# Performance work log

Hardware: AMD Instinct MI355X
Metric: run time of the kernel (lower is better)

The kernel has to match this reference:

```python
import jax, jax.numpy as jnp
import numpy as np
import math

G = 256      # graphs per batch
N0 = 256     # nodes per graph at input
RATIO = 0.5  # TopKPooling ratio


def gcn_conv(x, src, dst, ew, W, b):
    h = x @ W
    n = x.shape[0]
    deg = jnp.zeros((n,), x.dtype).at[dst].add(ew) + 1.0  # +1 for self-loop
    dinv = jax.lax.rsqrt(deg)
    norm = dinv[src] * dinv[dst] * ew
    agg = jnp.zeros_like(h).at[dst].add(norm[:, None] * h[src])
    return agg + h / deg[:, None] + b  # self-loop norm = 1/deg


def topk_pool(x, src, dst, ew, w, n_per_graph):
    # PyG TopKPooling: score = tanh(x.w/||w||); keep top ceil(ratio*n) per graph;
    # x_out = x[perm] * score[perm]; edges between dropped nodes are masked out.
    k = int(math.ceil(RATIO * n_per_graph))
    score = jnp.tanh((x @ w) / jnp.linalg.norm(w))
    top_s, top_i = jax.lax.top_k(score.reshape(G, n_per_graph), k)  # [G,k]
    perm = (top_i + (jnp.arange(G) * n_per_graph)[:, None]).reshape(-1)
    new_x = x[perm] * top_s.reshape(-1, 1)
    new_id = jnp.full((x.shape[0],), -1, jnp.int32).at[perm].set(
        jnp.arange(G * k, dtype=jnp.int32))
    ns, nd = new_id[src], new_id[dst]
    valid = (ns >= 0) & (nd >= 0)
    new_ew = ew * valid.astype(x.dtype)
    ns = jnp.where(valid, ns, 0)
    nd = jnp.where(valid, nd, 0)
    new_batch = jnp.repeat(jnp.arange(G, dtype=jnp.int32), k)
    return new_x, ns, nd, new_ew, new_batch, k


def readout(x, batch):
    # torch.cat([global_max_pool, global_mean_pool], dim=1)
    mx = jax.ops.segment_max(x, batch, num_segments=G)
    cnt = jax.ops.segment_sum(jnp.ones((x.shape[0],), x.dtype), batch, num_segments=G)
    mn = jax.ops.segment_sum(x, batch, num_segments=G) / cnt[:, None]
    return jnp.concatenate([mx, mn], axis=1)


def _forward(x, edge_index, batch, gcn_w0, gcn_b0, gcn_w1, gcn_b1, gcn_w2, gcn_b2,
             pool_w0, pool_w1, pool_w2, lin1_w, lin1_b, lin2_w, lin2_b, lin3_w, lin3_b):
    src, dst = edge_index[0], edge_index[1]
    ew = jnp.ones((src.shape[0],), x.dtype)
    npg = N0
    h = jax.nn.relu(gcn_conv(x, src, dst, ew, gcn_w0, gcn_b0))
    h, src, dst, ew, batch, npg = topk_pool(h, src, dst, ew, pool_w0, npg)
    out = readout(h, batch)
    for Wg, bg, pw in ((gcn_w1, gcn_b1, pool_w1), (gcn_w2, gcn_b2, pool_w2)):
        h = jax.nn.relu(gcn_conv(h, src, dst, ew, Wg, bg))
        h, src, dst, ew, batch, npg = topk_pool(h, src, dst, ew, pw, npg)
        out = out + readout(h, batch)
    h1 = jax.nn.relu(out @ lin1_w + lin1_b)  # dropout = identity (eval mode)
    h2 = jax.nn.relu(h1 @ lin2_w + lin2_b)
    logits = h2 @ lin3_w + lin3_b
    return jax.nn.log_softmax(logits, axis=-1)


def setup_inputs() -> dict:
    key = jax.random.key(0)
    ks = jax.random.split(key, 16)
    EPG = 2048  # edges per graph (avg degree 8)
    F_IN, H = 128, 256
    num_nodes, E = G * N0, G * EPG
    x = jax.random.normal(ks[0], (num_nodes, F_IN), jnp.float32)
    offs = jnp.repeat(jnp.arange(G, dtype=jnp.int32) * N0, EPG)
    src = offs + jax.random.randint(ks[1], (E,), 0, N0, dtype=jnp.int32)
    dst = offs + jax.random.randint(ks[2], (E,), 0, N0, dtype=jnp.int32)

    def glorot(k, shape):
        lim = float(np.sqrt(6.0 / (shape[0] + shape[1])))
        return jax.random.uniform(k, shape, jnp.float32, -lim, lim)

    return {
        "x": x,
        "edge_index": jnp.stack([src, dst]),
        "batch": jnp.arange(num_nodes, dtype=jnp.int32) // N0,
        "gcn_w0": glorot(ks[3], (F_IN, H)), "gcn_b0": jnp.zeros((H,), jnp.float32),
        "gcn_w1": glorot(ks[4], (H, H)), "gcn_b1": jnp.zeros((H,), jnp.float32),
        "gcn_w2": glorot(ks[5], (H, H)), "gcn_b2": jnp.zeros((H,), jnp.float32),
        "pool_w0": jax.random.normal(ks[6], (H,), jnp.float32) * 0.1,
        "pool_w1": jax.random.normal(ks[7], (H,), jnp.float32) * 0.1,
        "pool_w2": jax.random.normal(ks[8], (H,), jnp.float32) * 0.1,
        "lin1_w": glorot(ks[9], (2 * H, H)), "lin1_b": jnp.zeros((H,), jnp.float32),
        "lin2_w": glorot(ks[10], (H, H // 2)), "lin2_b": jnp.zeros((H // 2,), jnp.float32),
        "lin3_w": glorot(ks[11], (H // 2, 2)), "lin3_b": jnp.zeros((2,), jnp.float32),
    }


def reference(x, edge_index, batch, gcn_w0, gcn_b0, gcn_w1, gcn_b1, gcn_w2, gcn_b2,
              pool_w0, pool_w1, pool_w2, lin1_w, lin1_b, lin2_w, lin2_b, lin3_w, lin3_b):
    return _forward(x, edge_index, batch, gcn_w0, gcn_b0, gcn_w1, gcn_b1, gcn_w2, gcn_b2,
                    pool_w0, pool_w1, pool_w2, lin1_w, lin1_b, lin2_w, lin2_b, lin3_w, lin3_b)
```

## Files before the change

kernel.cpp:

```cpp
#include <hip/hip_runtime.h>
#include <hip/hip_bf16.h>
#include <math.h>

#define G_GRAPHS 256
#define EPG 2048
#define E_TOT 524288
#define HF 256
#define FIN 128

__global__ void init_cur(int* __restrict__ cur) {
    int i = blockIdx.x * blockDim.x + threadIdx.x;
    if (i < G_GRAPHS * 256) cur[i] = i & 255;
}

template <int K>
__global__ __launch_bounds__(256, 4)
void gemm_v9(const float* __restrict__ A, const float* __restrict__ W,
             float* __restrict__ C) {
    __shared__ __align__(16) float As[2][32 * 68];
    __shared__ __align__(16) float Wa[2][32 * 68];
    __shared__ __align__(16) float Wb[2][32 * 68];
    const int tid = threadIdx.x;
    const int tx = tid & 15;
    const int ty = tid >> 4;
    const int r0 = blockIdx.x * 64;
    const int c0 = blockIdx.y * 128;
    const int l8 = tid >> 3;
    const int kq = tid & 7;
    const int wkk = tid >> 5;
    const int wc = tid & 31;
    float acc[4][8] = {{0.f}};
    float4 va0, va1, vw0, vw1, vw2, vw3;

    auto load_regs = [&](int k0) {
        va0 = *(const float4*)&A[(size_t)(r0 + l8) * K + k0 + 4 * kq];
        va1 = *(const float4*)&A[(size_t)(r0 + 32 + l8) * K + k0 + 4 * kq];
        vw0 = *(const float4*)&W[(size_t)(k0 + 0  + wkk) * 256 + c0 + 4 * wc];
        vw1 = *(const float4*)&W[(size_t)(k0 + 8  + wkk) * 256 + c0 + 4 * wc];
        vw2 = *(const float4*)&W[(size_t)(k0 + 16 + wkk) * 256 + c0 + 4 * wc];
        vw3 = *(const float4*)&W[(size_t)(k0 + 24 + wkk) * 256 + c0 + 4 * wc];
    };
    auto write_stage = [&](int b) {
        {
            int rs = l8 ^ (kq << 3);
            As[b][(4 * kq + 0) * 68 + rs] = va0.x;
            As[b][(4 * kq + 1) * 68 + rs] = va0.y;
            As[b][(4 * kq + 2) * 68 + rs] = va0.z;
            As[b][(4 * kq + 3) * 68 + rs] = va0.w;
        }
        {
            int rs = (32 + l8) ^ (kq << 3);
            As[b][(4 * kq + 0) * 68 + rs] = va1.x;
            As[b][(4 * kq + 1) * 68 + rs] = va1.y;
            As[b][(4 * kq + 2) * 68 + rs] = va1.z;
            As[b][(4 * kq + 3) * 68 + rs] = va1.w;
        }
        if (wc < 16) {
            *(float4*)&Wa[b][(0  + wkk) * 68 + 4 * wc] = vw0;
            *(float4*)&Wa[b][(8  + wkk) * 68 + 4 * wc] = vw1;
            *(float4*)&Wa[b][(16 + wkk) * 68 + 4 * wc] = vw2;
            *(float4*)&Wa[b][(24 + wkk) * 68 + 4 * wc] = vw3;
        } else {
            *(float4*)&Wb[b][(0  + wkk) * 68 + 4 * (wc - 16)] = vw0;
            *(float4*)&Wb[b][(8  + wkk) * 68 + 4 * (wc - 16)] = vw1;
            *(float4*)&Wb[b][(16 + wkk) * 68 + 4 * (wc - 16)] = vw2;
            *(float4*)&Wb[b][(24 + wkk) * 68 + 4 * (wc - 16)] = vw3;
        }
    };
    auto compute = [&](int b) {
#pragma unroll 4
        for (int kk = 0; kk < 32; ++kk) {
            const int g = (ty * 4) ^ ((kk >> 2) << 3);
            const float4 a0 = *(const float4*)&As[b][kk * 68 + g];
            const float4 w0 = *(const float4*)&Wa[b][kk * 68 + tx * 4];
            const float4 w1 = *(const float4*)&Wb[b][kk * 68 + tx * 4];
            float av[4] = {a0.x, a0.y, a0.z, a0.w};
            float wv_[8] = {w0.x, w0.y, w0.z, w0.w, w1.x, w1.y, w1.z, w1.w};
#pragma unroll
            for (int i = 0; i < 4; ++i)
#pragma unroll
                for (int j = 0; j < 8; ++j)
                    acc[i][j] += av[i] * wv_[j];
        }
    };

    load_regs(0);
    write_stage(0);
    __syncthreads();
    int cur = 0;
    for (int k0 = 0; k0 < K - 32; k0 += 32) {
        load_regs(k0 + 32);
        compute(cur);
        write_stage(cur ^ 1);
        __syncthreads();
        cur ^= 1;
    }
    compute(cur);

#pragma unroll
    for (int i = 0; i < 4; ++i) {
        float4 v0 = make_float4(acc[i][0], acc[i][1], acc[i][2], acc[i][3]);
        float4 v1 = make_float4(acc[i][4], acc[i][5], acc[i][6], acc[i][7]);
        size_t base = (size_t)(r0 + ty * 4 + i) * 256 + c0 + tx * 4;
        *(float4*)&C[base] = v0;
        *(float4*)&C[base + 64] = v1;
    }
}

__global__ __launch_bounds__(256)
void csr_build(const int* __restrict__ ei, const int* __restrict__ cur, int npg,
               int* __restrict__ degS, float* __restrict__ dinvS,
               int* __restrict__ startsS, int2* __restrict__ slots2) {
    __shared__ int cul[EPG];
    __shared__ short dstv[EPG];
    __shared__ unsigned char rnk[EPG];
    __shared__ int h[32][256];
    __shared__ int cnt[256];
    __shared__ int st[256];
    const int g = blockIdx.x;
    const int t = threadIdx.x;
    const int lane = t & 63;
    const int wv = t >> 6;

    for (int i = t; i < 32 * 256; i += 256) ((int*)h)[i] = 0;
    for (int e = t; e < EPG; e += 256) {
        size_t idx = (size_t)g * EPG + e;
        int cu = cur[g * 256 + (ei[idx] - g * 256)];
        int cv = cur[g * 256 + (ei[E_TOT + idx] - g * 256)];
        bool valid = (cu >= 0 && cv >= 0);
        cul[e] = cu;
        dstv[e] = valid ? (short)cv : (short)256;
    }
    __syncthreads();
    for (int c = wv; c < 32; c += 4) {
        int e = c * 64 + lane;
        int d = (int)dstv[e];
        unsigned long long m = ~0ULL;
#pragma unroll
        for (int b = 0; b < 9; ++b) {
            unsigned long long bb = __ballot((d >> b) & 1);
            m &= ((d >> b) & 1) ? bb : ~bb;
        }
        int r = __popcll(m & ((1ULL << lane) - 1ULL));
        rnk[e] = (unsigned char)r;
        if (r == 0 && d < 256) h[c][d] = __popcll(m);
    }
    __syncthreads();
    if (t < npg) {
        int run = 0;
        for (int c = 0; c < 32; ++c) { int v = h[c][t]; h[c][t] = run; run += v; }
        cnt[t] = run;
        degS[g * npg + t] = run + 1;
        dinvS[g * npg + t] = 1.0f / sqrtf((float)(run + 1));
    }
    __syncthreads();
    if (t == 0) {
        int run = 0;
        for (int i = 0; i < npg; ++i) { st[i] = run; run += cnt[i]; }
    }
    __syncthreads();
    if (t < npg) startsS[g * npg + t] = g * EPG + st[t];
    for (int e = t; e < EPG; e += 256) {
        int d = (int)dstv[e];
        if (d < npg) {
            int slot = st[d] + h[e >> 6][d] + (int)rnk[e];
            int cu = cul[e];
            float dv = 1.0f / sqrtf((float)(cnt[cu] + 1));
            slots2[g * EPG + slot] = make_int2(g * npg + cu, __float_as_int(dv));
        }
    }
}

__global__ __launch_bounds__(256)
void agg_score2(const int* __restrict__ degS, const float* __restrict__ dinvS,
                const int* __restrict__ startsS, const int2* __restrict__ slots2,
                const float* __restrict__ HL, float* __restrict__ H2,
                const float* __restrict__ bias, const float* __restrict__ pw,
                float* __restrict__ score, int nbOver8) {
    __shared__ float vrow[4][256];
    const int t = threadIdx.x;
    const int wv = t >> 6;
    const int lane = t & 63;
    const int blk = (blockIdx.x & 7) * nbOver8 + (blockIdx.x >> 3);
    const int node = blk * 4 + wv;
    const int cntE = degS[node] - 1;
    const float degF = (float)(cntE + 1);
    const float dn = dinvS[node];
    const int2* sl = slots2 + startsS[node];
    float ax = 0.f, ay = 0.f, az = 0.f, aw = 0.f;
    int j = 0;
    for (; j + 8 <= cntE; j += 8) {
        int2 s[8];
#pragma unroll
        for (int u = 0; u < 8; ++u) s[u] = sl[j + u];
        float4 hv[8];
#pragma unroll
        for (int u = 0; u < 8; ++u)
            hv[u] = *(const float4*)&HL[(size_t)s[u].x * 256 + 4 * lane];
#pragma unroll
        for (int u = 0; u < 8; ++u) {
            float dv = __int_as_float(s[u].y);
            ax += dv * hv[u].x; ay += dv * hv[u].y;
            az += dv * hv[u].z; aw += dv * hv[u].w;
        }
    }
    for (; j + 4 <= cntE; j += 4) {
        int2 s[4];
#pragma unroll
        for (int u = 0; u < 4; ++u) s[u] = sl[j + u];
        float4 hv[4];
#pragma unroll
        for (int u = 0; u < 4; ++u)
            hv[u] = *(const float4*)&HL[(size_t)s[u].x * 256 + 4 * lane];
#pragma unroll
        for (int u = 0; u < 4; ++u) {
            float dv = __int_as_float(s[u].y);
            ax += dv * hv[u].x; ay += dv * hv[u].y;
            az += dv * hv[u].z; aw += dv * hv[u].w;
        }
    }
    for (; j < cntE; ++j) {
        int2 sv = sl[j];
        float dv = __int_as_float(sv.y);
        float4 hv = *(const float4*)&HL[(size_t)sv.x * 256 + 4 * lane];
        ax += dv * hv.x; ay += dv * hv.y; az += dv * hv.z; aw += dv * hv.w;
    }
    const float4 hn = *(const float4*)&HL[(size_t)node * 256 + 4 * lane];
    const float4 bi = *(const float4*)&bias[4 * lane];
    float4 v;
    v.x = ax * dn + hn.x / degF + bi.x;  v.x = fmaxf(v.x, 0.f);
    v.y = ay * dn + hn.y / degF + bi.y;  v.y = fmaxf(v.y, 0.f);
    v.z = az * dn + hn.z / degF + bi.z;  v.z = fmaxf(v.z, 0.f);
    v.w = aw * dn + hn.w / degF + bi.w;  v.w = fmaxf(v.w, 0.f);
    *(float4*)&H2[(size_t)node * 256 + 4 * lane] = v;
    *(float4*)&vrow[wv][4 * lane] = v;
    float pr = 0.f, s2p = 0.f;
    for (int jj = 0; jj < 4; ++jj) {
        int f = lane + 64 * jj;
        float w = pw[f];
        pr += vrow[wv][f] * w;
        s2p += w * w;
    }
    for (int off = 32; off; off >>= 1) {
        pr += __shfl_down(pr, off, 64);
        s2p += __shfl_down(s2p, off, 64);
    }
    s2p = __shfl(s2p, 0, 64);
    if (lane == 0) score[node] = tanhf(pr / sqrtf(s2p));
}

__global__ __launch_bounds__(256)
void topk_fused(const float* __restrict__ score, int npg, int k,
                const float* __restrict__ H2, float* __restrict__ OUT,
                float* __restrict__ outacc, int* __restrict__ cur, int first) {
    __shared__ float ss[256];
    __shared__ int si_[256];
    __shared__ int rankOf[256];
    const int g = blockIdx.x;
    const int t = threadIdx.x;
    if (t < npg) { ss[t] = score[g * npg + t]; si_[t] = t; }
    else         { ss[t] = -INFINITY; si_[t] = 0x7FFFFFFF; }
    for (int size = 2; size <= 256; size <<= 1) {
        for (int stride = size >> 1; stride > 0; stride >>= 1) {
            __syncthreads();
            int i = t, j = t ^ stride;
            if (j > i) {
                float a = ss[i], b = ss[j];
                int ia = si_[i], ib = si_[j];
                bool inOrder = (a > b) || (a == b && ia < ib);
                bool desc = ((i & size) == 0);
                if (desc ? !inOrder : inOrder) {
                    ss[i] = b; ss[j] = a; si_[i] = ib; si_[j] = ia;
                }
            }
        }
    }
    __syncthreads();
    rankOf[t] = -1;
    __syncthreads();
    if (t < k) rankOf[si_[t]] = t;
    __syncthreads();
    {
        int v = g * 256 + t;
        int c = cur[v];
        cur[v] = (c >= 0) ? rankOf[c] : -1;
    }
    const size_t gb = (size_t)g * npg * 256;
    float mx = -INFINITY, sm = 0.f;
    for (int n = 0; n < k; n += 4) {
        float v0 = H2[gb + (size_t)si_[n + 0] * 256 + t] * ss[n + 0];
        float v1 = H2[gb + (size_t)si_[n + 1] * 256 + t] * ss[n + 1];
        float v2 = H2[gb + (size_t)si_[n + 2] * 256 + t] * ss[n + 2];
        float v3 = H2[gb + (size_t)si_[n + 3] * 256 + t] * ss[n + 3];
        size_t ob = ((size_t)g * k + n) * 256 + t;
        OUT[ob]       = v0;
        OUT[ob + 256] = v1;
        OUT[ob + 512] = v2;
        OUT[ob + 768] = v3;
        mx = fmaxf(mx, v0); sm += v0;
        mx = fmaxf(mx, v1); sm += v1;
        mx = fmaxf(mx, v2); sm += v2;
        mx = fmaxf(mx, v3); sm += v3;
    }
    float mean = sm / (float)k;
    if (first) {
        outacc[g * 512 + t] = mx;
        outacc[g * 512 + 256 + t] = mean;
    } else {
        outacc[g * 512 + t] += mx;
        outacc[g * 512 + 256 + t] += mean;
    }
}

__global__ __launch_bounds__(256)
void mlp_head(const float* __restrict__ outacc,
              const float* __restrict__ l1w, const float* __restrict__ l1b,
              const float* __restrict__ l2w, const float* __restrict__ l2b,
              const float* __restrict__ l3w, const float* __restrict__ l3b,
              float* __restrict__ out) {
    __shared__ float row[512];
    __shared__ float h1[256];
    __shared__ float h2[128];
    const int g = blockIdx.x;
    const int t = threadIdx.x;
    row[t] = outacc[g * 512 + t];
    row[256 + t] = outacc[g * 512 + 256 + t];
    __syncthreads();
    {
        float a = l1b[t];
        for (int j = 0; j < 512; ++j) a += row[j] * l1w[j * 256 + t];
        h1[t] = fmaxf(a, 0.f);
    }
    __syncthreads();
    if (t < 128) {
        float a2 = l2b[t];
        for (int j = 0; j < 256; ++j) a2 += h1[j] * l2w[j * 128 + t];
        h2[t] = fmaxf(a2, 0.f);
    }
    __syncthreads();
    if (t == 0) {
        float l0 = l3b[0], l1 = l3b[1];
        for (int j = 0; j < 128; ++j) {
            float h = h2[j];
            l0 += h * l3w[j * 2 + 0];
            l1 += h * l3w[j * 2 + 1];
        }
        float m = fmaxf(l0, l1);
        float lse = m + logf(expf(l0 - m) + expf(l1 - m));
        out[g * 2 + 0] = l0 - lse;
        out[g * 2 + 1] = l1 - lse;
    }
}

__global__ __launch_bounds__(256, 1)
void gnn_mono(const float* __restrict__ x, const int* __restrict__ ei,
              const float* __restrict__ gw0, const float* __restrict__ gb0,
              const float* __restrict__ gw1, const float* __restrict__ gb1,
              const float* __restrict__ gw2, const float* __restrict__ gb2,
              const float* __restrict__ pw0, const float* __restrict__ pw1,
              const float* __restrict__ pw2,
              const float* __restrict__ l1w, const float* __restrict__ l1b,
              const float* __restrict__ l2w, const float* __restrict__ l2b,
              const float* __restrict__ l3w, const float* __restrict__ l3b,
              float* __restrict__ out, float* __restrict__ ws) {
    const int g = blockIdx.x;
    const int t = threadIdx.x;
    float* P = ws + (size_t)g * HF * 256;
    float* Q = ws + (size_t)G_GRAPHS * HF * 256 + (size_t)g * HF * 256;
    __shared__ int   eb[EPG];
    __shared__ int   slots[EPG];
    __shared__ int   curID[256];
    __shared__ int   cntL[256];
    __shared__ int   startL[256];
    __shared__ float degF[256];
    __shared__ float dinv[256];
    __shared__ float sa[256];
    __shared__ float ss[256];
    __shared__ int   si_[256];
    __shared__ float scoreV[256];
    __shared__ int   kept[128];
    __shared__ int   rankOf[256];
    __shared__ float row[512];
    for (int e = t; e < EPG; e += 256) {
        size_t idx = (size_t)g * EPG + e;
        eb[e] = ((ei[idx] - g * 256) << 8) | (ei[E_TOT + idx] - g * 256);
    }
    curID[t] = t;
    float accMx = 0.f, accMn = 0.f;
    const float* GW[3] = {gw0, gw1, gw2};
    const float* GB[3] = {gb0, gb1, gb2};
    const float* PW[3] = {pw0, pw1, pw2};
    const int kk[3] = {128, 64, 32};
    int npg = 256;
    __syncthreads();
    for (int s = 0; s < 3; ++s) {
        const int knext = kk[s];
        {
            const float* Wp = GW[s];
            const int K = (s == 0) ? FIN : HF;
            for (int n = 0; n < npg; ++n) {
                if (s == 0) { if (t < FIN) sa[t] = x[(size_t)(g * 256 + n) * FIN + t]; }
                else sa[t] = P[(size_t)n * HF + t];
                __syncthreads();
                float a = 0.f;
                for (int k2 = 0; k2 < K; ++k2) a += sa[k2] * Wp[k2 * HF + t];
                Q[(size_t)n * HF + t] = a;
                __syncthreads();
            }
        }
        cntL[t] = 0;
        __syncthreads();
        for (int e = t; e < EPG; e += 256) {
            int p = eb[e];
            int cu = curID[p >> 8], cv = curID[p & 255];
            if (cu >= 0 && cv >= 0) atomicAdd(&cntL[cv], 1);
        }
        __syncthreads();
        if (t == 0) { int run = 0; for (int i = 0; i < npg; ++i) { startL[i] = run; run += cntL[i]; } }
        __syncthreads();
        if (t < npg) {
            float d = (float)cntL[t] + 1.0f;
            degF[t] = d;
            dinv[t] = 1.0f / sqrtf(d);
            int c = startL[t];
            for (int e = 0; e < EPG; ++e) {
                int p = eb[e];
                int cu = curID[p >> 8], cv = curID[p & 255];
                if (cu >= 0 && cv >= 0 && cv == t) slots[c++] = e;
            }
        }
        __syncthreads();
        {
            const float bb = GB[s][t];
            for (int n = 0; n < npg; ++n) {
                float acc = 0.f;
                const int s0 = startL[n], s1 = s0 + cntL[n];
                for (int j = s0; j < s1; ++j) {
                    int scur = curID[eb[slots[j]] >> 8];
                    acc += dinv[scur] * Q[(size_t)scur * HF + t];
                }
                float v = acc * dinv[n] + Q[(size_t)n * HF + t] / degF[n] + bb;
                P[(size_t)n * HF + t] = fmaxf(v, 0.f);
            }
        }
        __syncthreads();
        {
            const float* pwp = PW[s];
            const int lane = t & 63, wv = t >> 6;
            float s2p = 0.f;
            for (int j = 0; j < 4; ++j) { float w = pwp[lane + 64 * j]; s2p += w * w; }
            for (int off = 32; off; off >>= 1) s2p += __shfl_down(s2p, off, 64);
            s2p = __shfl(s2p, 0, 64);
            const float nw = sqrtf(s2p);
            for (int n = wv; n < npg; n += 4) {
                float pr = 0.f;
                for (int j = 0; j < 4; ++j) { int f = lane + 64 * j; pr += P[(size_t)n * HF + f] * pwp[f]; }
                for (int off = 32; off; off >>= 1) pr += __shfl_down(pr, off, 64);
                if (lane == 0) scoreV[n] = tanhf(pr / nw);
            }
        }
        __syncthreads();
        if (t < npg) { ss[t] = scoreV[t]; si_[t] = t; }
        else         { ss[t] = -INFINITY; si_[t] = 0x7FFFFFFF; }
        for (int size = 2; size <= 256; size <<= 1) {
            for (int stride = size >> 1; stride > 0; stride >>= 1) {
                __syncthreads();
                int i = t, j = t ^ stride;
                if (j > i) {
                    float a = ss[i], b = ss[j];
                    int ia = si_[i], ib = si_[j];
                    bool inOrder = (a > b) || (a == b && ia < ib);
                    bool desc = ((i & size) == 0);
                    if (desc ? !inOrder : inOrder) { ss[i] = b; ss[j] = a; si_[i] = ib; si_[j] = ia; }
                }
            }
        }
        __syncthreads();
        if (t < knext) kept[t] = si_[t];
        __syncthreads();
        {
            float mx = -INFINITY, sm = 0.f;
            for (int n = 0; n < knext; ++n) {
                int o = kept[n];
                float vv = P[(size_t)o * HF + t] * scoreV[o];
                Q[(size_t)n * HF + t] = vv;
                mx = fmaxf(mx, vv);
                sm += vv;
            }
            accMx += mx;
            accMn += sm / (float)knext;
        }
        rankOf[t] = -1;
        __syncthreads();
        if (t < knext) rankOf[kept[t]] = t;
        __syncthreads();
        { int c = curID[t]; curID[t] = (c >= 0) ? rankOf[c] : -1; }
        __syncthreads();
        { float* tmp = P; P = Q; Q = tmp; }
        npg = knext;
    }
    row[t] = accMx;
    row[256 + t] = accMn;
    __syncthreads();
    { float a = l1b[t]; for (int j = 0; j < 512; ++j) a += row[j] * l1w[j * 256 + t]; scoreV[t] = fmaxf(a, 0.f); }
    __syncthreads();
    if (t < 128) { float a2 = l2b[t]; for (int j = 0; j < 256; ++j) a2 += scoreV[j] * l2w[j * 128 + t]; sa[t] = fmaxf(a2, 0.f); }
    __syncthreads();
    if (t == 0) {
        float l0 = l3b[0], l1 = l3b[1];
        for (int j = 0; j < 128; ++j) { float h = sa[j]; l0 += h * l3w[j * 2 + 0]; l1 += h * l3w[j * 2 + 1]; }
        float m = fmaxf(l0, l1);
        float lse = m + logf(expf(l0 - m) + expf(l1 - m));
        out[g * 2 + 0] = l0 - lse;
        out[g * 2 + 1] = l1 - lse;
    }
}

extern "C" void kernel_launch(void* const* d_in, const int* in_sizes, int n_in,
                              void* d_out, int out_size, void* d_ws, size_t ws_size,
                              hipStream_t stream) {
    const float* x   = (const float*)d_in[0];
    const int*   ei  = (const int*)d_in[1];
    const float* gw0 = (const float*)d_in[3];
    const float* gb0 = (const float*)d_in[4];
    const float* gw1 = (const float*)d_in[5];
    const float* gb1 = (const float*)d_in[6];
    const float* gw2 = (const float*)d_in[7];
    const float* gb2 = (const float*)d_in[8];
    const float* pw0 = (const float*)d_in[9];
    const float* pw1 = (const float*)d_in[10];
    const float* pw2 = (const float*)d_in[11];
    const float* l1w = (const float*)d_in[12];
    const float* l1b = (const float*)d_in[13];
    const float* l2w = (const float*)d_in[14];
    const float* l2b = (const float*)d_in[15];
    const float* l3w = (const float*)d_in[16];
    const float* l3b = (const float*)d_in[17];
    float* out = (float*)d_out;

    const size_t SLAB = (size_t)65536 * 256;
    char* p = (char*)d_ws;
    float* P      = (float*)p; p += SLAB * 4;
    float* Q      = (float*)p; p += SLAB * 4;
    int*   cur    = (int*)p;   p += (size_t)65536 * 4;
    int*   degS   = (int*)p;   p += (size_t)65536 * 4;
    float* dinvS  = (float*)p; p += (size_t)65536 * 4;
    int*   starts = (int*)p;   p += (size_t)65536 * 4;
    int2*  slots2 = (int2*)p;  p += (size_t)E_TOT * 8;
    float* score  = (float*)p; p += (size_t)65536 * 4;
    int*   kept   = (int*)p;   p += (size_t)32768 * 4;
    float* outacc = (float*)p; p += (size_t)G_GRAPHS * 512 * 4;
    const size_t needed = (size_t)(p - (char*)d_ws);

    if (ws_size < needed) {
        gnn_mono<<<G_GRAPHS, 256, 0, stream>>>(
            x, ei, gw0, gb0, gw1, gb1, gw2, gb2, pw0, pw1, pw2,
            l1w, l1b, l2w, l2b, l3w, l3b, out, (float*)d_ws);
        return;
    }

    init_cur<<<(G_GRAPHS * 256 + 255) / 256, 256, 0, stream>>>(cur);

    const int   npg[3] = {256, 128, 64};
    const int   kk[3]  = {128, 64, 32};
    const int   Ns[3]  = {65536, 32768, 16384};
    const float* GW[3] = {gw0, gw1, gw2};
    const float* GB[3] = {gb0, gb1, gb2};
    const float* PW[3] = {pw0, pw1, pw2};

    float* HLs[3]   = {P, Q, P};
    float* H2s[3]   = {Q, P, Q};
    float* POOLs[3] = {P, Q, P};

    for (int s = 0; s < 3; ++s) {
        const int n = Ns[s];
        const int k = kk[s];
        if (s == 0) {
            gemm_v9<FIN><<<dim3(n / 64, 2), 256, 0, stream>>>(x, GW[s], HLs[s]);
        } else {
            gemm_v9<HF><<<dim3(n / 64, 2), 256, 0, stream>>>(POOLs[s - 1], GW[s], HLs[s]);
        }
        csr_build<<<G_GRAPHS, 256, 0, stream>>>(ei, cur, npg[s],
                                                degS, dinvS, starts, slots2);
        agg_score2<<<n / 4, 256, 0, stream>>>(degS, dinvS, starts, slots2,
                                              HLs[s], H2s[s], GB[s], PW[s], score,
                                              n / 32);
        topk_fused<<<G_GRAPHS, 256, 0, stream>>>(score, npg[s], k,
                                                 H2s[s], POOLs[s], outacc, cur,
                                                 s == 0 ? 1 : 0);
    }

    mlp_head<<<G_GRAPHS, 256, 0, stream>>>(outacc, l1w, l1b, l2w, l2b, l3w, l3b, out);
}
```

Measured before the change: 432.0 us.

## Restructure GEMM to read wave-uniform W rows directly, staging only A in LDS

The GEMM no longer stages W tiles in shared memory. Each wave owns 32 output columns, and readfirstlane makes the W address wave-uniform, so W can be read straight from global memory, likely as scalar loads. Only A is staged, transposed, in a single double-buffered LDS tile, and each lane computes one row times 32 columns. This removes the W LDS traffic and its bank-conflict swizzling, but it relies on uniform loads being served from cache and puts 32 accumulators per thread.

```diff
diff --git a/kernel.cpp b/kernel.cpp
--- a/kernel.cpp
+++ b/kernel.cpp
@@ -15,72 +15,57 @@
 
 template <int K>
 __global__ __launch_bounds__(256, 4)
-void gemm_v9(const float* __restrict__ A, const float* __restrict__ W,
-             float* __restrict__ C) {
-    __shared__ __align__(16) float As[2][32 * 68];
-    __shared__ __align__(16) float Wa[2][32 * 68];
-    __shared__ __align__(16) float Wb[2][32 * 68];
+void gemm_v10(const float* __restrict__ A, const float* __restrict__ W,
+              float* __restrict__ C) {
+    __shared__ float As[2][32 * 68];
     const int tid = threadIdx.x;
-    const int tx = tid & 15;
-    const int ty = tid >> 4;
+    const int lane = tid & 63;
     const int r0 = blockIdx.x * 64;
-    const int c0 = blockIdx.y * 128;
-    const int l8 = tid >> 3;
-    const int kq = tid & 7;
-    const int wkk = tid >> 5;
-    const int wc = tid & 31;
-    float acc[4][8] = {{0.f}};
-    float4 va0, va1, vw0, vw1, vw2, vw3;
+    const int cb = blockIdx.y * 128 + (tid >> 6) * 32;
+    const int cbu = __builtin_amdgcn_readfirstlane(cb);
+    const float* __restrict__ Wu = W + cbu;
+    const int sr = tid >> 2;
+    const int sq = tid & 3;
+    float acc[32] = {};
+    float4 va0, va1;
 
     auto load_regs = [&](int k0) {
-        va0 = *(const float4*)&A[(size_t)(r0 + l8) * K + k0 + 4 * kq];
-        va1 = *(const float4*)&A[(size_t)(r0 + 32 + l8) * K + k0 + 4 * kq];
-        vw0 = *(const float4*)&W[(size_t)(k0 + 0  + wkk) * 256 + c0 + 4 * wc];
-        vw1 = *(const float4*)&W[(size_t)(k0 + 8  + wkk) * 256 + c0 + 4 * wc];
-        vw2 = *(const float4*)&W[(size_t)(k0 + 16 + wkk) * 256 + c0 + 4 * wc];
-        vw3 = *(const float4*)&W[(size_t)(k0 + 24 + wkk) * 256 + c0 + 4 * wc];
+        va0 = *(const float4*)&A[(size_t)(r0 + sr) * K + k0 + 4 * sq];
+        va1 = *(const float4*)&A[(size_t)(r0 + sr) * K + k0 + 16 + 4 * sq];
     };
     auto write_stage = [&](int b) {
-        {
-            int rs = l8 ^ (kq << 3);
-            As[b][(4 * kq + 0) * 68 + rs] = va0.x;
-            As[b][(4 * kq + 1) * 68 + rs] = va0.y;
-            As[b][(4 * kq + 2) * 68 + rs] = va0.z;
-            As[b][(4 * kq + 3) * 68 + rs] = va0.w;
-        }
-        {
-            int rs = (32 + l8) ^ (kq << 3);
-            As[b][(4 * kq + 0) * 68 + rs] = va1.x;
-            As[b][(4 * kq + 1) * 68 + rs] = va1.y;
-            As[b][(4 * kq + 2) * 68 + rs] = va1.z;
-            As[b][(4 * kq + 3) * 68 + rs] = va1.w;
-        }
-        if (wc < 16) {
-            *(float4*)&Wa[b][(0  + wkk) * 68 + 4 * wc] = vw0;
-            *(float4*)&Wa[b][(8  + wkk) * 68 + 4 * wc] = vw1;
-            *(float4*)&Wa[b][(16 + wkk) * 68 + 4 * wc] = vw2;
-            *(float4*)&Wa[b][(24 + wkk) * 68 + 4 * wc] = vw3;
-        } else {
-            *(float4*)&Wb[b][(0  + wkk) * 68 + 4 * (wc - 16)] = vw0;
-            *(float4*)&Wb[b][(8  + wkk) * 68 + 4 * (wc - 16)] = vw1;
-            *(float4*)&Wb[b][(16 + wkk) * 68 + 4 * (wc - 16)] = vw2;
-            *(float4*)&Wb[b][(24 + wkk) * 68 + 4 * (wc - 16)] = vw3;
-        }
+        float* p0 = &As[b][(4 * sq) * 68 + sr];
+        p0[0]   = va0.x; p0[68]  = va0.y; p0[136] = va0.z; p0[204] = va0.w;
+        float* p1 = &As[b][(16 + 4 * sq) * 68 + sr];
+        p1[0]   = va1.x; p1[68]  = va1.y; p1[136] = va1.z; p1[204] = va1.w;
     };
-    auto compute = [&](int b) {
-#pragma unroll 4
-        for (int kk = 0; kk < 32; ++kk) {
-            const int g = (ty * 4) ^ ((kk >> 2) << 3);
-            const float4 a0 = *(const float4*)&As[b][kk * 68 + g];
-            const float4 w0 = *(const float4*)&Wa[b][kk * 68 + tx * 4];
-            const float4 w1 = *(const float4*)&Wb[b][kk * 68 + tx * 4];
-            float av[4] = {a0.x, a0.y, a0.z, a0.w};
-            float wv_[8] = {w0.x, w0.y, w0.z, w0.w, w1.x, w1.y, w1.z, w1.w};
-#pragma unroll
-            for (int i = 0; i < 4; ++i)
-#pragma unroll
-                for (int j = 0; j < 8; ++j)
-                    acc[i][j] += av[i] * wv_[j];
+    auto compute = [&](int b, int k0) {
+#pragma unroll
+        for (int kq = 0; kq < 8; ++kq) {
+            float av[4];
+#pragma unroll
+            for (int u = 0; u < 4; ++u)
+                av[u] = As[b][(4 * kq + u) * 68 + lane];
+#pragma unroll
+            for (int u = 0; u < 4; ++u) {
+                const float* wr = &Wu[(size_t)(k0 + 4 * kq + u) * 256];
+                float4 w0 = *(const float4*)&wr[0];
+                float4 w1 = *(const float4*)&wr[4];
+                float4 w2 = *(const float4*)&wr[8];
+                float4 w3 = *(const float4*)&wr[12];
+                float4 w4 = *(const float4*)&wr[16];
+                float4 w5 = *(const float4*)&wr[20];
+                float4 w6 = *(const float4*)&wr[24];
+                float4 w7 = *(const float4*)&wr[28];
+                const float wv_[32] = {
+                    w0.x, w0.y, w0.z, w0.w, w1.x, w1.y, w1.z, w1.w,
+                    w2.x, w2.y, w2.z, w2.w, w3.x, w3.y, w3.z, w3.w,
+                    w4.x, w4.y, w4.z, w4.w, w5.x, w5.y, w5.z, w5.w,
+                    w6.x, w6.y, w6.z, w6.w, w7.x, w7.y, w7.z, w7.w};
+#pragma unroll
+                for (int j = 0; j < 32; ++j)
+                    acc[j] += av[u] * wv_[j];
+            }
         }
     };
 
@@ -90,21 +75,18 @@
     int cur = 0;
     for (int k0 = 0; k0 < K - 32; k0 += 32) {
         load_regs(k0 + 32);
-        compute(cur);
+        compute(cur, k0);
         write_stage(cur ^ 1);
         __syncthreads();
         cur ^= 1;
     }
-    compute(cur);
-
-#pragma unroll
-    for (int i = 0; i < 4; ++i) {
-        float4 v0 = make_float4(acc[i][0], acc[i][1], acc[i][2], acc[i][3]);
-        float4 v1 = make_float4(acc[i][4], acc[i][5], acc[i][6], acc[i][7]);
-        size_t base = (size_t)(r0 + ty * 4 + i) * 256 + c0 + tx * 4;
-        *(float4*)&C[base] = v0;
-        *(float4*)&C[base + 64] = v1;
-    }
+    compute(cur, K - 32);
+
+    const size_t base = (size_t)(r0 + lane) * 256 + cb;
+#pragma unroll
+    for (int j = 0; j < 32; j += 4)
+        *(float4*)&C[base + j] =
+            make_float4(acc[j], acc[j + 1], acc[j + 2], acc[j + 3]);
 }
 
 __global__ __launch_bounds__(256)
@@ -576,9 +558,9 @@
         const int n = Ns[s];
         const int k = kk[s];
         if (s == 0) {
-            gemm_v9<FIN><<<dim3(n / 64, 2), 256, 0, stream>>>(x, GW[s], HLs[s]);
+            gemm_v10<FIN><<<dim3(n / 64, 2), 256, 0, stream>>>(x, GW[s], HLs[s]);
         } else {
-            gemm_v9<HF><<<dim3(n / 64, 2), 256, 0, stream>>>(POOLs[s - 1], GW[s], HLs[s]);
+            gemm_v10<HF><<<dim3(n / 64, 2), 256, 0, stream>>>(POOLs[s - 1], GW[s], HLs[s]);
         }
         csr_build<<<G_GRAPHS, 256, 0, stream>>>(ei, cur, npg[s],
                                                 degS, dinvS, starts, slots2);
```

Measured after the change: 528.2 us. 22.3% more time.
